# Performance work log

Hardware: AMD Instinct MI355X
Metric: run time of the kernel (lower is better)

The kernel has to match this reference:

```python
import jax, jax.numpy as jnp
import numpy as np

N_DIM = 1024   # nodes (rows of s, rows of Kweight)
IN_DIM = 1024  # nodes / feature dim (cols of s, rows of Qweight, side of Gmat)
H_DIM = 64
B = 16


def setup_inputs() -> dict:
    key = jax.random.key(0)
    k1, k2, k3, k4 = jax.random.split(key, 4)
    s = jax.random.normal(k1, (N_DIM, B, IN_DIM), dtype=jnp.float32)
    Gmat = jax.random.uniform(k2, (IN_DIM, IN_DIM), dtype=jnp.float32)
    # torch init: rand * (4/d)**0.5 - (1/d)**0.5  => U[-(1/d)**0.5, (1/d)**0.5]... kept faithful
    Qweight = jax.random.uniform(k3, (IN_DIM, H_DIM), dtype=jnp.float32) * (4.0 / IN_DIM) ** 0.5 - (1.0 / IN_DIM) ** 0.5
    Kweight = jax.random.uniform(k4, (N_DIM, H_DIM), dtype=jnp.float32) * (4.0 / N_DIM) ** 0.5 - (1.0 / N_DIM) ** 0.5
    return {"s": s, "Gmat": Gmat, "Qweight": Qweight, "Kweight": Kweight}


def reference(s, Gmat, Qweight, Kweight):
    h_dim = Qweight.shape[1]
    inv_sqrt_h = 1.0 / jnp.sqrt(jnp.float32(h_dim))
    # q: einsum('ijk,km->ijm', s, Qw).permute(1,0,2) -> (B, n, h)
    q = jnp.einsum('nbi,ih->bnh', s, Qweight)
    # k: s.permute(1,2,0) einsum Kw then permute(0,2,1) -> (B, h, i)
    k = jnp.einsum('nbi,nh->bhi', s, Kweight)
    # squared (non-softmax) attention scores: (B, n, i)
    att = jnp.square(jnp.einsum('bnh,bhi->bni', q, k) * inv_sqrt_h + 1e-9)
    # adjacency aggregation: (B, n, i) @ (i, i)
    att = jnp.einsum('bni,ij->bnj', att, Gmat)
    # row-normalize and permute back to (n, B, i)
    s_t = jnp.sum(att, axis=2, keepdims=True) + 0.001
    return (att / s_t).transpose(1, 0, 2)
```

## Files before the change

### kernel.cpp

```cpp
#include <hip/hip_runtime.h>
#include <hip/hip_bf16.h>
#include <stdint.h>

typedef unsigned short u16;
typedef unsigned int   u32;

#define N_DIM  1024
#define IN_DIM 1024
#define H_DIM  64
#define BATCH  16

typedef __bf16 bf16x8 __attribute__((ext_vector_type(8)));
typedef float  f32x4  __attribute__((ext_vector_type(4)));

__device__ inline u16 f2bf(float f) {
    union { float f; u32 u; } v; v.f = f;
    u32 u = v.u;
    return (u16)((u + 0x7fffu + ((u >> 16) & 1u)) >> 16);
}
__device__ inline u32 pack2(float a, float b) {
    __hip_bfloat162 h = __float22bfloat162_rn(float2{a, b});
    union { __hip_bfloat162 h; u32 u; } cv; cv.h = h; return cv.u;
}

__device__ inline void gl_lds16(const u16* g, u16* l) {
    __builtin_amdgcn_global_load_lds(
        (const __attribute__((address_space(1))) u32*)g,
        (__attribute__((address_space(3))) u32*)l, 16, 0, 0);
}

__global__ void prep_w(const float* __restrict__ Q, const float* __restrict__ Kw,
                       u16* __restrict__ QT, u16* __restrict__ KwT) {
    int idx = blockIdx.x * 256 + threadIdx.x;
    const float* src = (idx < 65536) ? Q : Kw;
    u16* dst = (idx < 65536) ? QT : KwT;
    int i = idx & 65535;
    int h = i >> 10;
    int n = i & 1023;
    dst[h * 1024 + n] = f2bf(src[n * 64 + h]);
}

__global__ void prep_g(const float* __restrict__ G, u16* __restrict__ Gbt,
                       float* __restrict__ Grsum) {
    __shared__ float tile[64][65];
    int i0 = blockIdx.y * 64, j0 = blockIdx.x * 64;
    int tx = threadIdx.x & 63, ty = threadIdx.x >> 6;
    for (int r = 0; r < 16; ++r) {
        int i = ty * 16 + r;
        tile[i][tx] = G[(size_t)(i0 + i) * 1024 + j0 + tx];
    }
    __syncthreads();
    for (int r = 0; r < 16; ++r) {
        int j = ty * 16 + r;
        Gbt[(size_t)(j0 + j) * 1024 + i0 + tx] = f2bf(tile[tx][j]);
    }
    if (ty == 0) {
        float sum = 0.f;
        for (int j = 0; j < 64; ++j) sum += tile[tx][j];
        atomicAdd(&Grsum[i0 + tx], sum);
    }
}

__global__ __launch_bounds__(256) void gemm_qkt(
        const float* __restrict__ s, const u16* __restrict__ QT,
        const u16* __restrict__ KwT, float* __restrict__ part) {
    int z = blockIdx.z; int b = z & 15; bool isq = (z < 16);
    int ks = blockIdx.y;
    int m0 = blockIdx.x * 128;
    __shared__ __align__(16) u16 As[128 * 40];
    __shared__ __align__(16) u16 Bs[64 * 40];
    const u16* Bt = isq ? QT : KwT;
    float* outp = part + (size_t)ks * 2097152 + (size_t)z * 65536;
    int t = threadIdx.x, lane = t & 63, w = t >> 6, quad = lane >> 4, l15 = lane & 15;
    f32x4 acc[2][4] = {};
    for (int kk = 0; kk < 8; ++kk) {
        int k0 = ks * 256 + kk * 32;
        {
            int h = t >> 2, c = (t & 3) * 8;
            uint4 v = *(const uint4*)&Bt[(size_t)h * 1024 + k0 + c];
            *(uint4*)&Bs[h * 40 + c] = v;
        }
        if (isq) {
            int r = t >> 1, c = (t & 1) * 16;
            const float* src = s + (size_t)(m0 + r) * (BATCH * IN_DIM) + (size_t)b * IN_DIM + k0 + c;
            float4 f0 = ((const float4*)src)[0];
            float4 f1 = ((const float4*)src)[1];
            float4 f2 = ((const float4*)src)[2];
            float4 f3 = ((const float4*)src)[3];
            uint4 w0 = { pack2(f0.x,f0.y), pack2(f0.z,f0.w), pack2(f1.x,f1.y), pack2(f1.z,f1.w) };
            uint4 w1 = { pack2(f2.x,f2.y), pack2(f2.z,f2.w), pack2(f3.x,f3.y), pack2(f3.z,f3.w) };
            *(uint4*)&As[r * 40 + c]     = w0;
            *(uint4*)&As[r * 40 + c + 8] = w1;
        } else {
            int nr = t >> 3, icb = (t & 7) * 4;
            const float* src = s + (size_t)(k0 + nr) * (BATCH * IN_DIM) + (size_t)b * IN_DIM + m0;
            for (int j3 = 0; j3 < 4; ++j3) {
                float4 f = *(const float4*)&src[icb + 32 * j3];
                As[(icb + 32*j3 + 0) * 40 + nr] = f2bf(f.x);
                As[(icb + 32*j3 + 1) * 40 + nr] = f2bf(f.y);
                As[(icb + 32*j3 + 2) * 40 + nr] = f2bf(f.z);
                As[(icb + 32*j3 + 3) * 40 + nr] = f2bf(f.w);
            }
        }
        __syncthreads();
        int kh = quad * 8;
        bf16x8 af[2], bfr[4];
        for (int rt = 0; rt < 2; ++rt) af[rt] = *(const bf16x8*)&As[(w*32 + rt*16 + l15) * 40 + kh];
        for (int ct = 0; ct < 4; ++ct) bfr[ct] = *(const bf16x8*)&Bs[(ct*16 + l15) * 40 + kh];
        for (int rt = 0; rt < 2; ++rt)
            for (int ct = 0; ct < 4; ++ct)
                acc[rt][ct] = __builtin_amdgcn_mfma_f32_16x16x32_bf16(af[rt], bfr[ct], acc[rt][ct], 0, 0, 0);
        __syncthreads();
    }
    for (int rt = 0; rt < 2; ++rt)
        for (int ct = 0; ct < 4; ++ct)
            for (int r = 0; r < 4; ++r) {
                int m = w * 32 + rt * 16 + quad * 4 + r;
                int n = ct * 16 + l15;
                outp[(size_t)(m0 + m) * 64 + n] = acc[rt][ct][r];
            }
}

__global__ void reduce_qkt(const float* __restrict__ part, u16* __restrict__ qkt_out) {
    int id = blockIdx.x * 256 + threadIdx.x;
    const float4* p = (const float4*)part;
    float4 a = p[id];
    float4 b1 = p[id + 524288];
    float4 c = p[id + 1048576];
    float4 d = p[id + 1572864];
    a.x += b1.x + c.x + d.x; a.y += b1.y + c.y + d.y;
    a.z += b1.z + c.z + d.z; a.w += b1.w + c.w + d.w;
    uint2 pk = { pack2(a.x, a.y), pack2(a.z, a.w) };
    ((uint2*)qkt_out)[id] = pk;
}

__global__ __launch_bounds__(256) void gemm_fused(
        const u16* __restrict__ qws, const u16* __restrict__ ktws,
        const u16* __restrict__ Gbt, const float* __restrict__ Grsum,
        float* __restrict__ out) {
    int b = blockIdx.z;
    int n0 = blockIdx.x * 128, m0 = blockIdx.y * 128;
    const u16* qb = qws  + (size_t)b * 65536;
    const u16* kb = ktws + (size_t)b * 65536;
    __shared__ __align__(16) u16 As[128 * 40];
    __shared__ __align__(16) u16 Bs[2][128 * 32];
    __shared__ __align__(16) u16 ktc[32 * 72];
    __shared__ __align__(16) float Grs[1024];
    __shared__ float rs[128];
    int t = threadIdx.x, lane = t & 63, w = t >> 6, quad = lane >> 4, l15 = lane & 15;
    int ti = w & 1;
    int wm = (w >> 1) * 64, wn = (w & 1) * 64;

    ((float4*)Grs)[t] = ((const float4*)Grsum)[t];
    if (t < 128) rs[t] = 0.f;

    bf16x8 qf[4][2];
    for (int j = 0; j < 4; ++j)
        for (int kick = 0; kick < 2; ++kick)
            qf[j][kick] = *(const bf16x8*)&qb[(size_t)(m0 + wm + j*16 + l15) * 64 + kick*32 + quad*8];

    int br = t >> 2, bc = (t & 3) * 8;
    int bsw = (br & 3) * 8;
    gl_lds16(Gbt + (size_t)(n0 + br) * 1024 + (bc ^ bsw),      &Bs[0][br * 32 + bc]);
    gl_lds16(Gbt + (size_t)(n0 + br + 64) * 1024 + (bc ^ bsw), &Bs[0][(br + 64) * 32 + bc]);
    int ir = t >> 3, ch = (t & 7) * 8;
    uint4 kreg = *(const uint4*)&kb[(size_t)ir * 64 + ch];

    f32x4 acc[4][4] = {};
    float partial[4] = {0.f, 0.f, 0.f, 0.f};

    for (int kk = 0; kk < 32; ++kk) {
        int buf = kk & 1;
        *(uint4*)&ktc[ir * 72 + ch] = kreg;
        __syncthreads();
        f32x4 sacc[4] = {};
        for (int kick = 0; kick < 2; ++kick) {
            bf16x8 ktf = *(const bf16x8*)&ktc[(ti*16 + l15) * 72 + kick*32 + quad*8];
            for (int j = 0; j < 4; ++j)
                sacc[j] = __builtin_amdgcn_mfma_f32_16x16x32_bf16(ktf, qf[j][kick], sacc[j], 0, 0, 0);
        }
        if (kk < 31)
            kreg = *(const uint4*)&kb[(size_t)((kk + 1) * 32 + ir) * 64 + ch];
        float4 g = *(const float4*)&Grs[kk * 32 + ti * 16 + quad * 4];
        for (int j = 0; j < 4; ++j) {
            float v0 = sacc[j][0] * 0.125f + 1e-9f; v0 *= v0;
            float v1 = sacc[j][1] * 0.125f + 1e-9f; v1 *= v1;
            float v2 = sacc[j][2] * 0.125f + 1e-9f; v2 *= v2;
            float v3 = sacc[j][3] * 0.125f + 1e-9f; v3 *= v3;
            partial[j] += v0 * g.x + v1 * g.y + v2 * g.z + v3 * g.w;
            uint2 pk = { pack2(v0, v1), pack2(v2, v3) };
            *(uint2*)&As[(wm + j*16 + l15) * 40 + ti*16 + quad*4] = pk;
        }
        __syncthreads();
        if (kk < 31) {
            gl_lds16(Gbt + (size_t)(n0 + br) * 1024 + (kk+1)*32 + (bc ^ bsw),      &Bs[buf^1][br * 32 + bc]);
            gl_lds16(Gbt + (size_t)(n0 + br + 64) * 1024 + (kk+1)*32 + (bc ^ bsw), &Bs[buf^1][(br + 64) * 32 + bc]);
        }
        int kh = quad * 8;
        bf16x8 af[4], bfr[4];
        for (int i = 0; i < 4; ++i) af[i]  = *(const bf16x8*)&As[(wm + i*16 + l15) * 40 + kh];
        for (int j = 0; j < 4; ++j) {
            int row = wn + j*16 + l15;
            bfr[j] = *(const bf16x8*)&Bs[buf][row * 32 + (kh ^ ((row & 3) * 8))];
        }
        for (int i = 0; i < 4; ++i)
            for (int j = 0; j < 4; ++j)
                acc[i][j] = __builtin_amdgcn_mfma_f32_16x16x32_bf16(af[i], bfr[j], acc[i][j], 0, 0, 0);
    }

    for (int j = 0; j < 4; ++j) {
        partial[j] += __shfl_xor(partial[j], 16, 64);
        partial[j] += __shfl_xor(partial[j], 32, 64);
    }
    if (quad == 0)
        for (int j = 0; j < 4; ++j) atomicAdd(&rs[wm + j*16 + l15], partial[j]);
    __syncthreads();
    if (t < 128) rs[t] = 1.0f / (rs[t] + 0.001f);
    __syncthreads();

    for (int i = 0; i < 4; ++i) {
        float4 rv = *(const float4*)&rs[wm + i * 16 + quad * 4];
        float rva[4] = { rv.x, rv.y, rv.z, rv.w };
        for (int r = 0; r < 4; ++r) {
            int m = m0 + wm + i * 16 + quad * 4 + r;
            float* orow = out + (size_t)m * (BATCH * IN_DIM) + (size_t)b * IN_DIM + n0;
            for (int j = 0; j < 4; ++j)
                orow[wn + j * 16 + l15] = acc[i][j][r] * rva[r];
        }
    }
}

extern "C" void kernel_launch(void* const* d_in, const int* in_sizes, int n_in,
                              void* d_out, int out_size, void* d_ws, size_t ws_size,
                              hipStream_t stream) {
    const float* s  = (const float*)d_in[0];
    const float* G  = (const float*)d_in[1];
    const float* Q  = (const float*)d_in[2];
    const float* Kw = (const float*)d_in[3];
    float* out = (float*)d_out;
    char* ws = (char*)d_ws;

    float* part  = (float*)(ws);
    u16*   qws   = (u16*)(ws + (size_t)(32u << 20));
    u16*   ktws  = qws + (size_t)16 * 65536;
    u16*   Gbt   = (u16*)(ws + (size_t)(36u << 20));
    u16*   QT    = (u16*)(ws + (size_t)(38u << 20));
    u16*   KwT   = (u16*)(ws + (size_t)(38u << 20) + (128u << 10));
    float* Grsum = (float*)(ws + (size_t)(38u << 20) + (256u << 10));

    hipMemsetAsync(Grsum, 0, 1024 * sizeof(float), stream);
    prep_w<<<512, 256, 0, stream>>>(Q, Kw, QT, KwT);
    prep_g<<<dim3(16, 16), 256, 0, stream>>>(G, Gbt, Grsum);
    gemm_qkt<<<dim3(8, 4, 32), 256, 0, stream>>>(s, QT, KwT, part);
    reduce_qkt<<<2048, 256, 0, stream>>>(part, qws);
    gemm_fused<<<dim3(8, 8, 16), 256, 0, stream>>>(qws, ktws, Gbt, Grsum, out);
}
```

Baseline: 229.8 us.

## Widen fused GEMM N-tile to 256 to halve recomputed attention scores

Each block of the fused kernel now covers 256 output columns instead of 128, with each wave computing a 64x128 accumulator tile. Because every block recomputes the squared QK^T scores for its m-tile, halving the number of n-tiles halves that redundant MFMA, exp-free elementwise and K-load work, and also halves the Grsum partial-sum work. The XOR swizzle on the G tile in shared memory is removed, and launch bounds request 2 blocks per CU. The cost is higher register and LDS pressure, fewer blocks (512), and possible LDS bank conflicts on B-fragment reads without the swizzle.

```diff
diff --git a/kernel.cpp b/kernel.cpp
--- a/kernel.cpp
+++ b/kernel.cpp
@@ -134,22 +134,23 @@
     ((uint2*)qkt_out)[id] = pk;
 }
 
-__global__ __launch_bounds__(256) void gemm_fused(
+__global__ __launch_bounds__(256, 2) void gemm_fused(
         const u16* __restrict__ qws, const u16* __restrict__ ktws,
         const u16* __restrict__ Gbt, const float* __restrict__ Grsum,
         float* __restrict__ out) {
     int b = blockIdx.z;
-    int n0 = blockIdx.x * 128, m0 = blockIdx.y * 128;
+    int n0 = blockIdx.x * 256, m0 = blockIdx.y * 128;
     const u16* qb = qws  + (size_t)b * 65536;
     const u16* kb = ktws + (size_t)b * 65536;
     __shared__ __align__(16) u16 As[128 * 40];
-    __shared__ __align__(16) u16 Bs[2][128 * 32];
+    __shared__ __align__(16) u16 Bs[2][256 * 32];
     __shared__ __align__(16) u16 ktc[32 * 72];
     __shared__ __align__(16) float Grs[1024];
     __shared__ float rs[128];
     int t = threadIdx.x, lane = t & 63, w = t >> 6, quad = lane >> 4, l15 = lane & 15;
     int ti = w & 1;
-    int wm = (w >> 1) * 64, wn = (w & 1) * 64;
+    int wm = (w >> 1) * 64;
+    int wn = (w & 1) * 128;
 
     ((float4*)Grs)[t] = ((const float4*)Grsum)[t];
     if (t < 128) rs[t] = 0.f;
@@ -160,13 +161,12 @@
             qf[j][kick] = *(const bf16x8*)&qb[(size_t)(m0 + wm + j*16 + l15) * 64 + kick*32 + quad*8];
 
     int br = t >> 2, bc = (t & 3) * 8;
-    int bsw = (br & 3) * 8;
-    gl_lds16(Gbt + (size_t)(n0 + br) * 1024 + (bc ^ bsw),      &Bs[0][br * 32 + bc]);
-    gl_lds16(Gbt + (size_t)(n0 + br + 64) * 1024 + (bc ^ bsw), &Bs[0][(br + 64) * 32 + bc]);
+    for (int g4 = 0; g4 < 4; ++g4)
+        gl_lds16(Gbt + (size_t)(n0 + br + g4*64) * 1024 + bc, &Bs[0][(br + g4*64) * 32 + bc]);
     int ir = t >> 3, ch = (t & 7) * 8;
     uint4 kreg = *(const uint4*)&kb[(size_t)ir * 64 + ch];
 
-    f32x4 acc[4][4] = {};
+    f32x4 acc[4][8] = {};
     float partial[4] = {0.f, 0.f, 0.f, 0.f};
 
     for (int kk = 0; kk < 32; ++kk) {
@@ -193,19 +193,21 @@
         }
         __syncthreads();
         if (kk < 31) {
-            gl_lds16(Gbt + (size_t)(n0 + br) * 1024 + (kk+1)*32 + (bc ^ bsw),      &Bs[buf^1][br * 32 + bc]);
-            gl_lds16(Gbt + (size_t)(n0 + br + 64) * 1024 + (kk+1)*32 + (bc ^ bsw), &Bs[buf^1][(br + 64) * 32 + bc]);
+            for (int g4 = 0; g4 < 4; ++g4)
+                gl_lds16(Gbt + (size_t)(n0 + br + g4*64) * 1024 + (kk+1)*32 + bc,
+                         &Bs[buf^1][(br + g4*64) * 32 + bc]);
         }
         int kh = quad * 8;
-        bf16x8 af[4], bfr[4];
-        for (int i = 0; i < 4; ++i) af[i]  = *(const bf16x8*)&As[(wm + i*16 + l15) * 40 + kh];
-        for (int j = 0; j < 4; ++j) {
-            int row = wn + j*16 + l15;
-            bfr[j] = *(const bf16x8*)&Bs[buf][row * 32 + (kh ^ ((row & 3) * 8))];
-        }
-        for (int i = 0; i < 4; ++i)
+        bf16x8 af[4];
+        for (int i = 0; i < 4; ++i) af[i] = *(const bf16x8*)&As[(wm + i*16 + l15) * 40 + kh];
+        for (int jh = 0; jh < 2; ++jh) {
+            bf16x8 bfr[4];
             for (int j = 0; j < 4; ++j)
-                acc[i][j] = __builtin_amdgcn_mfma_f32_16x16x32_bf16(af[i], bfr[j], acc[i][j], 0, 0, 0);
+                bfr[j] = *(const bf16x8*)&Bs[buf][(wn + jh*64 + j*16 + l15) * 32 + kh];
+            for (int i = 0; i < 4; ++i)
+                for (int j = 0; j < 4; ++j)
+                    acc[i][jh*4 + j] = __builtin_amdgcn_mfma_f32_16x16x32_bf16(af[i], bfr[j], acc[i][jh*4 + j], 0, 0, 0);
+        }
     }
 
     for (int j = 0; j < 4; ++j) {
@@ -223,9 +225,9 @@
         float rva[4] = { rv.x, rv.y, rv.z, rv.w };
         for (int r = 0; r < 4; ++r) {
             int m = m0 + wm + i * 16 + quad * 4 + r;
-            float* orow = out + (size_t)m * (BATCH * IN_DIM) + (size_t)b * IN_DIM + n0;
-            for (int j = 0; j < 4; ++j)
-                orow[wn + j * 16 + l15] = acc[i][j][r] * rva[r];
+            float* orow = out + (size_t)m * (BATCH * IN_DIM) + (size_t)b * IN_DIM + n0 + wn;
+            for (int j = 0; j < 8; ++j)
+                orow[j * 16 + l15] = acc[i][j][r] * rva[r];
         }
     }
 }
@@ -253,5 +255,5 @@
     prep_g<<<dim3(16, 16), 256, 0, stream>>>(G, Gbt, Grsum);
     gemm_qkt<<<dim3(8, 4, 32), 256, 0, stream>>>(s, QT, KwT, part);
     reduce_qkt<<<2048, 256, 0, stream>>>(part, qws);
-    gemm_fused<<<dim3(8, 8, 16), 256, 0, stream>>>(qws, ktws, Gbt, Grsum, out);
-}
+    gemm_fused<<<dim3(4, 8, 16), 256, 0, stream>>>(qws, ktws, Gbt, Grsum, out);
+}
```

Result: faster. 193.4 us (-15.9%).
